# Kernel optimization log

Hardware: AMD Instinct MI355X
Metric: run time of the kernel (lower is better)

Reference implementation:

```python
import jax, jax.numpy as jnp
import numpy as np

N_NODES = 100000
N_EDGES = 600000
D = 128
L = 4
BN_EPS = 1e-5


def setup_inputs() -> dict:
    key = jax.random.key(0)
    ks = jax.random.split(key, 12)
    x = jax.random.normal(ks[0], (N_NODES, D), dtype=jnp.float32)
    edge_index = jax.random.randint(ks[1], (2, N_EDGES), 0, N_NODES, dtype=jnp.int64)
    edge_attr = jax.random.uniform(ks[2], (N_EDGES, 1), dtype=jnp.float32)
    s = 0.05
    return {
        'x': x,
        'edge_index': edge_index,
        'edge_attr': edge_attr,
        'We': jax.random.normal(ks[3], (L, 1, D), dtype=jnp.float32) * s,   # GINE edge projection Linear(1, D)
        'be': jnp.zeros((L, D), dtype=jnp.float32),
        'eps': jnp.zeros((L,), dtype=jnp.float32),                          # train_eps=True, init 0
        'W1': jax.random.normal(ks[4], (L, D, D), dtype=jnp.float32) * s,
        'b1': jnp.zeros((L, D), dtype=jnp.float32),
        'gamma': jnp.ones((L, D), dtype=jnp.float32),
        'beta': jnp.zeros((L, D), dtype=jnp.float32),
        'W2': jax.random.normal(ks[5], (L, D, D), dtype=jnp.float32) * s,
        'b2': jnp.zeros((L, D), dtype=jnp.float32),
    }


def _gine_layer(h, src, dst, edge_attr, We, be, eps, W1, b1, gamma, beta, W2, b2):
    n = h.shape[0]
    e = edge_attr @ We + be                       # [E, D] edge embedding
    m = jax.nn.relu(h[src] + e)                   # gather + add + relu (messages)
    agg = jax.ops.segment_sum(m, dst, num_segments=n)  # scatter-add to destination nodes
    z = (1.0 + eps) * h + agg
    # MLP: Linear -> BatchNorm1d (training stats) -> ReLU -> Linear
    z = z @ W1 + b1
    mu = jnp.mean(z, axis=0)
    var = jnp.var(z, axis=0)                      # biased var, as in torch BN training
    z = (z - mu) * jax.lax.rsqrt(var + BN_EPS) * gamma + beta
    z = jax.nn.relu(z)
    return z @ W2 + b2


def reference(x, edge_index, edge_attr, We, be, eps, W1, b1, gamma, beta, W2, b2):
    src, dst = edge_index[0], edge_index[1]
    h = x
    for l in range(L):
        z = _gine_layer(h, src, dst, edge_attr, We[l], be[l], eps[l],
                        W1[l], b1[l], gamma[l], beta[l], W2[l], b2[l])
        r = jax.nn.relu(z)
        h = r if l == 0 else h + r
    return h
```

## Files before the change

kernel.cpp:

```cpp
#include <hip/hip_runtime.h>

#define NN 100000
#define NE 600000
#define DD 128
#define NL 4
#define GB 512

typedef __attribute__((ext_vector_type(8))) short short8;
typedef __attribute__((ext_vector_type(4))) float float4v;

__device__ inline unsigned short f2bf(float f) {
  union { float f; unsigned u; } v; v.f = f;
  unsigned r = v.u + 0x7fff + ((v.u >> 16) & 1);
  return (unsigned short)(r >> 16);
}
__device__ inline float bf2f(unsigned short u) {
  union { unsigned u; float f; } v; v.u = ((unsigned)u) << 16;
  return v.f;
}

__global__ void k_prep(const float* __restrict__ W1, const float* __restrict__ W2,
                       unsigned short* __restrict__ WT, int* __restrict__ counts,
                       float* __restrict__ stats4) {
  int i = blockIdx.x * 256 + threadIdx.x;
  if (i < NN) counts[i] = 0;
  if (i < NL * 256) stats4[i] = 0.f;
  if (i >= 8 * 16384) return;
  int m = i >> 14;
  int el = i & 16383;
  int k = el >> 7;
  int n = el & 127;
  const float* src = (m < 4) ? (W1 + (size_t)m * 16384) : (W2 + (size_t)(m - 4) * 16384);
  WT[(size_t)m * 16384 + n * 128 + k] = f2bf(src[k * 128 + n]);
}

__global__ void k_h2b(const float* __restrict__ src, unsigned short* __restrict__ dst,
                      const int* __restrict__ ei, int* __restrict__ counts) {
  int i = blockIdx.x * 256 + threadIdx.x;
  if (i < NE) atomicAdd(&counts[ei[NE + i]], 1);
  if (i >= NN * DD / 4) return;
  float4 v = ((const float4*)src)[i];
  ushort4 o;
  o.x = f2bf(v.x); o.y = f2bf(v.y); o.z = f2bf(v.z); o.w = f2bf(v.w);
  ((ushort4*)dst)[i] = o;
}

#define ST 256
#define SC 2
#define SB ((NN + ST * SC - 1) / (ST * SC))

__global__ void k_scan_part(const int* __restrict__ counts, int* __restrict__ row_ptr,
                            int* __restrict__ bsums) {
  __shared__ int s[ST];
  int b = blockIdx.x, t = threadIdx.x;
  int base = b * (ST * SC) + t * SC;
  int v0 = (base < NN) ? counts[base] : 0;
  int v1 = (base + 1 < NN) ? counts[base + 1] : 0;
  int tsum = v0 + v1;
  s[t] = tsum;
  __syncthreads();
  for (int d = 1; d < ST; d <<= 1) {
    int x = (t >= d) ? s[t - d] : 0;
    __syncthreads();
    s[t] += x;
    __syncthreads();
  }
  int excl = s[t] - tsum;
  if (base < NN) row_ptr[base] = excl;
  if (base + 1 < NN) row_ptr[base + 1] = excl + v0;
  if (t == ST - 1) bsums[b] = s[t];
}

__global__ void k_scan_bsum(const int* __restrict__ bsums, int* __restrict__ boffs,
                            int* __restrict__ row_ptr) {
  __shared__ int s[ST];
  int t = threadIdx.x;
  int v = (t < SB) ? bsums[t] : 0;
  s[t] = v;
  __syncthreads();
  for (int d = 1; d < ST; d <<= 1) {
    int x = (t >= d) ? s[t - d] : 0;
    __syncthreads();
    s[t] += x;
    __syncthreads();
  }
  if (t < SB) boffs[t] = s[t] - v;
  if (t == ST - 1) row_ptr[NN] = s[t];
}

__global__ void k_scan_add(const int* __restrict__ boffs, int* __restrict__ row_ptr,
                           int* __restrict__ off) {
  int b = blockIdx.x, t = threadIdx.x;
  int base = b * (ST * SC) + t * SC;
  int o = boffs[b];
  if (base < NN) { row_ptr[base] += o; off[base] = 0; }
  if (base + 1 < NN) { row_ptr[base + 1] += o; off[base + 1] = 0; }
}

__global__ void k_fill(const int* __restrict__ ei, const float* __restrict__ attr,
                       const int* __restrict__ row_ptr, int* __restrict__ off,
                       int2* __restrict__ csr) {
  int e = blockIdx.x * 256 + threadIdx.x;
  if (e >= NE) return;
  int srcv = ei[e];
  int dstv = ei[NE + e];
  int pos = atomicAdd(&off[dstv], 1);
  int idx = row_ptr[dstv] + pos;
  csr[idx] = make_int2(srcv, __float_as_int(attr[e]));
}

#define CONSUME(hv, a)                                                                   \
  do {                                                                                   \
    acc0.x += fmaxf(__uint_as_float((hv).x << 16)          + fmaf((a), we0.x, be0.x), 0.f); \
    acc0.y += fmaxf(__uint_as_float((hv).x & 0xffff0000u)  + fmaf((a), we0.y, be0.y), 0.f); \
    acc0.z += fmaxf(__uint_as_float((hv).y << 16)          + fmaf((a), we0.z, be0.z), 0.f); \
    acc0.w += fmaxf(__uint_as_float((hv).y & 0xffff0000u)  + fmaf((a), we0.w, be0.w), 0.f); \
    acc1.x += fmaxf(__uint_as_float((hv).z << 16)          + fmaf((a), we1.x, be1.x), 0.f); \
    acc1.y += fmaxf(__uint_as_float((hv).z & 0xffff0000u)  + fmaf((a), we1.y, be1.y), 0.f); \
    acc1.z += fmaxf(__uint_as_float((hv).w << 16)          + fmaf((a), we1.z, be1.z), 0.f); \
    acc1.w += fmaxf(__uint_as_float((hv).w & 0xffff0000u)  + fmaf((a), we1.w, be1.w), 0.f); \
  } while (0)

__global__ void k_agg(const unsigned short* __restrict__ hb,
                      const int* __restrict__ row_ptr, const int2* __restrict__ csr,
                      const float* __restrict__ We, const float* __restrict__ be,
                      const float* __restrict__ epsp, unsigned short* __restrict__ zb) {
  int gid = blockIdx.x * blockDim.x + threadIdx.x;
  int n = gid >> 4;
  int li = gid & 15;
  if (n >= NN) return;
  int d0 = li * 8;
  float4 we0 = *(const float4*)(We + d0);
  float4 we1 = *(const float4*)(We + d0 + 4);
  float4 be0 = *(const float4*)(be + d0);
  float4 be1 = *(const float4*)(be + d0 + 4);
  int b = row_ptr[n], e = row_ptr[n + 1];
  int deg = e - b;
  int cnt = (deg < 16) ? deg : 16;
  int2 rec = (li < cnt) ? csr[b + li] : make_int2(0, 0);
  int myidx = rec.x;
  float myatt = __int_as_float(rec.y);

  float4 acc0 = make_float4(0.f, 0.f, 0.f, 0.f);
  float4 acc1 = make_float4(0.f, 0.f, 0.f, 0.f);

  int i = 0;
  for (; i + 4 <= cnt; i += 4) {
    int s0 = __shfl(myidx, i, 16);
    int s1 = __shfl(myidx, i + 1, 16);
    int s2 = __shfl(myidx, i + 2, 16);
    int s3 = __shfl(myidx, i + 3, 16);
    float a0 = __shfl(myatt, i, 16);
    float a1 = __shfl(myatt, i + 1, 16);
    float a2 = __shfl(myatt, i + 2, 16);
    float a3 = __shfl(myatt, i + 3, 16);
    uint4 hv0 = *(const uint4*)(hb + (size_t)s0 * DD + d0);
    uint4 hv1 = *(const uint4*)(hb + (size_t)s1 * DD + d0);
    uint4 hv2 = *(const uint4*)(hb + (size_t)s2 * DD + d0);
    uint4 hv3 = *(const uint4*)(hb + (size_t)s3 * DD + d0);
    CONSUME(hv0, a0);
    CONSUME(hv1, a1);
    CONSUME(hv2, a2);
    CONSUME(hv3, a3);
  }
  for (; i < cnt; i++) {
    int s = __shfl(myidx, i, 16);
    float a = __shfl(myatt, i, 16);
    uint4 hv = *(const uint4*)(hb + (size_t)s * DD + d0);
    CONSUME(hv, a);
  }
  for (int j = b + 16; j < e; j++) {
    int2 r2 = csr[j];
    float a = __int_as_float(r2.y);
    uint4 hv = *(const uint4*)(hb + (size_t)r2.x * DD + d0);
    CONSUME(hv, a);
  }

  float ep = 1.f + epsp[0];
  uint4 hs = *(const uint4*)(hb + (size_t)n * DD + d0);
  float z0 = fmaf(ep, __uint_as_float(hs.x << 16), acc0.x);
  float z1 = fmaf(ep, __uint_as_float(hs.x & 0xffff0000u), acc0.y);
  float z2 = fmaf(ep, __uint_as_float(hs.y << 16), acc0.z);
  float z3 = fmaf(ep, __uint_as_float(hs.y & 0xffff0000u), acc0.w);
  float z4 = fmaf(ep, __uint_as_float(hs.z << 16), acc1.x);
  float z5 = fmaf(ep, __uint_as_float(hs.z & 0xffff0000u), acc1.y);
  float z6 = fmaf(ep, __uint_as_float(hs.w << 16), acc1.z);
  float z7 = fmaf(ep, __uint_as_float(hs.w & 0xffff0000u), acc1.w);
  uint4 o;
  o.x = (unsigned)f2bf(z0) | ((unsigned)f2bf(z1) << 16);
  o.y = (unsigned)f2bf(z2) | ((unsigned)f2bf(z3) << 16);
  o.z = (unsigned)f2bf(z4) | ((unsigned)f2bf(z5) << 16);
  o.w = (unsigned)f2bf(z6) | ((unsigned)f2bf(z7) << 16);
  *(uint4*)(zb + (size_t)n * DD + d0) = o;
}

template <int MODE>
__global__ __launch_bounds__(256, 2) void k_gemm(
    const unsigned short* __restrict__ Xb, const unsigned short* __restrict__ WT,
    const float* __restrict__ bias, float* __restrict__ stats,
    const float* __restrict__ gamma, const float* __restrict__ beta,
    const float* __restrict__ hprev, float* __restrict__ Yout,
    unsigned short* __restrict__ Ybf) {
  __shared__ unsigned short Wl[128 * 136];
  __shared__ unsigned short Xl[2][64 * 136];
  __shared__ float bns[256];
  const int tid = threadIdx.x;
  const int G = gridDim.x;
  const int NT = (NN + 63) >> 6;

  for (int i = tid; i < 2048; i += 256) {
    int rr = i >> 4, c = i & 15;
    *(uint4*)&Wl[rr * 136 + c * 8] = *(const uint4*)&WT[rr * 128 + c * 8];
  }

  const int lane = tid & 63;
  const int w = tid >> 6;
  const int m = lane & 15;
  const int quad = lane >> 4;

  const int c8 = tid & 15, rr16 = tid >> 4;
  float scl[8], sfl[8];
  if (MODE >= 1) {
    if (tid < 128) {
      const float invN = 1.f / (float)NN;
      float mu = stats[tid] * invN;
      float var = fmaxf(stats[128 + tid] * invN - mu * mu, 0.f);
      float xx = var + 1e-5f;
      float r = rsqrtf(xx);
      r = r * (1.5f - 0.5f * xx * r * r);
      float scale = gamma[tid] * r;
      bns[tid] = scale;
      bns[128 + tid] = beta[tid] - mu * scale;
    }
    __syncthreads();
#pragma unroll
    for (int j = 0; j < 8; j++) {
      scl[j] = bns[c8 * 8 + j];
      sfl[j] = bns[128 + c8 * 8 + j];
    }
  }

  uint4 xu[4];
  auto LOADR = [&](int t) {
    int r0 = t << 6;
#pragma unroll
    for (int it = 0; it < 4; it++) {
      int gr = r0 + rr16 + it * 16;
      xu[it] = (gr < NN) ? *(const uint4*)(Xb + (size_t)gr * DD + c8 * 8)
                         : make_uint4(0u, 0u, 0u, 0u);
    }
  };
  auto STORE_LDS = [&](int b) {
#pragma unroll
    for (int it = 0; it < 4; it++) {
      int row = rr16 + it * 16;
      uint4 u = xu[it];
      if (MODE >= 1) {
        unsigned p[4] = {u.x, u.y, u.z, u.w};
#pragma unroll
        for (int j = 0; j < 4; j++) {
          float lo = bf2f((unsigned short)(p[j] & 0xffffu));
          float hi = bf2f((unsigned short)(p[j] >> 16));
          lo = fmaxf(fmaf(lo, scl[2 * j], sfl[2 * j]), 0.f);
          hi = fmaxf(fmaf(hi, scl[2 * j + 1], sfl[2 * j + 1]), 0.f);
          p[j] = (unsigned)f2bf(lo) | ((unsigned)f2bf(hi) << 16);
        }
        u = make_uint4(p[0], p[1], p[2], p[3]);
      }
      *(uint4*)&Xl[b][row * 136 + c8 * 8] = u;
    }
  };

  float4v ssum[8], ssq[8];
  if (MODE == 0) {
#pragma unroll
    for (int ct = 0; ct < 8; ct++) {
      ssum[ct] = (float4v){0.f, 0.f, 0.f, 0.f};
      ssq[ct] = (float4v){0.f, 0.f, 0.f, 0.f};
    }
  }

  const int t0 = blockIdx.x;
  LOADR(t0);
  STORE_LDS(0);
  if (t0 + G < NT) LOADR(t0 + G);
  __syncthreads();

  int buf = 0;
  for (int t = t0; t < NT; t += G) {
    const int nxt = t + G;
    if (nxt < NT) {
      STORE_LDS(buf ^ 1);
      if (nxt + G < NT) LOADR(nxt + G);
    }

    float4v acc[8];
#pragma unroll
    for (int ct = 0; ct < 8; ct++) {
      float4 b4 = *(const float4*)&bias[ct * 16 + quad * 4];
      acc[ct] = (float4v){b4.x, b4.y, b4.z, b4.w};
    }

    const unsigned short* Ap = &Wl[m * 136 + quad * 8];
    const unsigned short* Bp = &Xl[buf][(w * 16 + m) * 136 + quad * 8];
#pragma unroll
    for (int q = 0; q < 4; q++) {
      short8 bfrag = *(const short8*)(Bp + q * 32);
#pragma unroll
      for (int ct = 0; ct < 8; ct++) {
        short8 afrag = *(const short8*)(Ap + ct * 16 * 136 + q * 32);
        acc[ct] = __builtin_amdgcn_mfma_f32_16x16x32_bf16(afrag, bfrag, acc[ct], 0, 0, 0);
      }
    }

    asm volatile("s_waitcnt lgkmcnt(0)" ::: "memory");
    __builtin_amdgcn_s_barrier();

    const int r = (t << 6) + w * 16 + m;
    if (r < NN) {
      const size_t rb = (size_t)r * DD;
#pragma unroll
      for (int ct = 0; ct < 8; ct++) {
        float4v v = acc[ct];
        const int col = ct * 16 + quad * 4;
        if (MODE == 0) {
          ssum[ct] += v;
          ssq[ct] += v * v;
          ushort4 o;
          o.x = f2bf(v[0]); o.y = f2bf(v[1]); o.z = f2bf(v[2]); o.w = f2bf(v[3]);
          *(ushort4*)&Ybf[rb + col] = o;
        } else {
          v[0] = fmaxf(v[0], 0.f); v[1] = fmaxf(v[1], 0.f);
          v[2] = fmaxf(v[2], 0.f); v[3] = fmaxf(v[3], 0.f);
          if (MODE == 2) {
            float4 hp = *(const float4*)&hprev[rb + col];
            v[0] += hp.x; v[1] += hp.y; v[2] += hp.z; v[3] += hp.w;
          }
          *(float4v*)&Yout[rb + col] = v;
          if (Ybf) {
            ushort4 o;
            o.x = f2bf(v[0]); o.y = f2bf(v[1]); o.z = f2bf(v[2]); o.w = f2bf(v[3]);
            *(ushort4*)&Ybf[rb + col] = o;
          }
        }
      }
    }
    buf ^= 1;
  }

  if (MODE == 0) {
    float* sarr = (float*)Xl;
    float* sqarr = sarr + 512;
#pragma unroll
    for (int ct = 0; ct < 8; ct++) {
      float4v s = ssum[ct], s2 = ssq[ct];
#pragma unroll
      for (int d = 1; d < 16; d <<= 1) {
#pragma unroll
        for (int j = 0; j < 4; j++) {
          s[j] += __shfl_xor(s[j], d);
          s2[j] += __shfl_xor(s2[j], d);
        }
      }
      if (m == 0) {
        *(float4v*)&sarr[w * 128 + ct * 16 + quad * 4] = s;
        *(float4v*)&sqarr[w * 128 + ct * 16 + quad * 4] = s2;
      }
    }
    __syncthreads();
    if (tid < 128) {
      atomicAdd(&stats[tid], sarr[tid] + sarr[128 + tid] + sarr[256 + tid] + sarr[384 + tid]);
    } else {
      int c = tid - 128;
      atomicAdd(&stats[128 + c], sqarr[c] + sqarr[128 + c] + sqarr[256 + c] + sqarr[384 + c]);
    }
  }
}

static inline size_t align256(size_t x) { return (x + 255) & ~(size_t)255; }

extern "C" void kernel_launch(void* const* d_in, const int* in_sizes, int n_in,
                              void* d_out, int out_size, void* d_ws, size_t ws_size,
                              hipStream_t stream) {
  const float* x     = (const float*)d_in[0];
  const int*   ei    = (const int*)d_in[1];
  const float* attr  = (const float*)d_in[2];
  const float* We    = (const float*)d_in[3];
  const float* be    = (const float*)d_in[4];
  const float* eps   = (const float*)d_in[5];
  const float* W1    = (const float*)d_in[6];
  const float* b1    = (const float*)d_in[7];
  const float* gamma = (const float*)d_in[8];
  const float* beta  = (const float*)d_in[9];
  const float* W2    = (const float*)d_in[10];
  const float* b2    = (const float*)d_in[11];
  float* out = (float*)d_out;

  char* w = (char*)d_ws;
  unsigned short* z2 = (unsigned short*)w; w += align256((size_t)NN * DD * 2);
  unsigned short* hb = (unsigned short*)w; w += align256((size_t)NN * DD * 2);
  unsigned short* zb = (unsigned short*)w; w += align256((size_t)NN * DD * 2);
  int*   row_ptr  = (int*)w;   w += align256((size_t)(NN + 1) * 4);
  int*   counts   = (int*)w;   w += align256((size_t)NN * 4);
  int*   off      = (int*)w;   w += align256((size_t)NN * 4);
  int2*  csr      = (int2*)w;  w += align256((size_t)NE * 8);
  float* stats4   = (float*)w; w += align256((size_t)NL * 256 * 4);
  int*   bsums    = (int*)w;   w += align256(ST * 4);
  int*   boffs    = (int*)w;   w += align256(ST * 4);
  unsigned short* WTb = (unsigned short*)w; w += align256((size_t)8 * 16384 * 2);

  k_prep<<<512, 256, 0, stream>>>(W1, W2, WTb, counts, stats4);
  k_h2b<<<(NN * DD / 4 + 255) / 256, 256, 0, stream>>>(x, hb, ei, counts);
  k_scan_part<<<SB, ST, 0, stream>>>(counts, row_ptr, bsums);
  k_scan_bsum<<<1, ST, 0, stream>>>(bsums, boffs, row_ptr);
  k_scan_add<<<SB, ST, 0, stream>>>(boffs, row_ptr, off);
  k_fill<<<(NE + 255) / 256, 256, 0, stream>>>(ei, attr, row_ptr, off, csr);

  for (int l = 0; l < NL; l++) {
    float* st = stats4 + (size_t)l * 256;
    k_agg<<<(NN * 16 + 255) / 256, 256, 0, stream>>>(
        hb, row_ptr, csr, We + l * DD, be + l * DD, eps + l, zb);
    k_gemm<0><<<GB, 256, 0, stream>>>(zb, WTb + (size_t)l * 16384, b1 + l * DD,
                                      st, nullptr, nullptr, nullptr, nullptr, z2);
    unsigned short* hbo = (l < NL - 1) ? hb : nullptr;
    if (l == 0)
      k_gemm<1><<<GB, 256, 0, stream>>>(z2, WTb + (size_t)(4 + l) * 16384, b2 + l * DD,
                                        st, gamma + l * DD, beta + l * DD,
                                        nullptr, out, hbo);
    else
      k_gemm<2><<<GB, 256, 0, stream>>>(z2, WTb + (size_t)(4 + l) * 16384, b2 + l * DD,
                                        st, gamma + l * DD, beta + l * DD,
                                        out, out, hbo);
  }
}
```

Baseline: 532.8 us.

## Make aggregation kernel grid-stride with prefetch of next node's CSR records

The aggregation kernel now launches a fixed grid of 1024 blocks and loops over nodes grid-stride, prefetching the next node's row pointers and first 16 CSR records while the current node's messages are consumed. The per-element math is rewritten with float2 vector ops to encourage packed FP32 instructions. Separately, the scan now seeds the offset array with row starts so the fill kernel uses the atomic result directly, dropping one row_ptr load. The risk is fewer resident waves hiding gather latency, since the grid is much smaller than one thread group per node.

```diff
diff --git a/kernel.cpp b/kernel.cpp
--- a/kernel.cpp
+++ b/kernel.cpp
@@ -8,6 +8,7 @@
 
 typedef __attribute__((ext_vector_type(8))) short short8;
 typedef __attribute__((ext_vector_type(4))) float float4v;
+typedef __attribute__((ext_vector_type(2))) float f2;
 
 __device__ inline unsigned short f2bf(float f) {
   union { float f; unsigned u; } v; v.f = f;
@@ -17,6 +18,12 @@
 __device__ inline float bf2f(unsigned short u) {
   union { unsigned u; float f; } v; v.u = ((unsigned)u) << 16;
   return v.f;
+}
+__device__ inline f2 bfpair(unsigned u) {
+  f2 r;
+  r.x = __uint_as_float(u << 16);
+  r.y = __uint_as_float(u & 0xffff0000u);
+  return r;
 }
 
 __global__ void k_prep(const float* __restrict__ W1, const float* __restrict__ W2,
@@ -93,105 +100,120 @@
   int b = blockIdx.x, t = threadIdx.x;
   int base = b * (ST * SC) + t * SC;
   int o = boffs[b];
-  if (base < NN) { row_ptr[base] += o; off[base] = 0; }
-  if (base + 1 < NN) { row_ptr[base + 1] += o; off[base + 1] = 0; }
+  if (base < NN) { int v = row_ptr[base] + o; row_ptr[base] = v; off[base] = v; }
+  if (base + 1 < NN) { int v = row_ptr[base + 1] + o; row_ptr[base + 1] = v; off[base + 1] = v; }
 }
 
 __global__ void k_fill(const int* __restrict__ ei, const float* __restrict__ attr,
-                       const int* __restrict__ row_ptr, int* __restrict__ off,
-                       int2* __restrict__ csr) {
+                       int* __restrict__ off, int2* __restrict__ csr) {
   int e = blockIdx.x * 256 + threadIdx.x;
   if (e >= NE) return;
   int srcv = ei[e];
   int dstv = ei[NE + e];
-  int pos = atomicAdd(&off[dstv], 1);
-  int idx = row_ptr[dstv] + pos;
+  int idx = atomicAdd(&off[dstv], 1);
   csr[idx] = make_int2(srcv, __float_as_int(attr[e]));
 }
 
-#define CONSUME(hv, a)                                                                   \
-  do {                                                                                   \
-    acc0.x += fmaxf(__uint_as_float((hv).x << 16)          + fmaf((a), we0.x, be0.x), 0.f); \
-    acc0.y += fmaxf(__uint_as_float((hv).x & 0xffff0000u)  + fmaf((a), we0.y, be0.y), 0.f); \
-    acc0.z += fmaxf(__uint_as_float((hv).y << 16)          + fmaf((a), we0.z, be0.z), 0.f); \
-    acc0.w += fmaxf(__uint_as_float((hv).y & 0xffff0000u)  + fmaf((a), we0.w, be0.w), 0.f); \
-    acc1.x += fmaxf(__uint_as_float((hv).z << 16)          + fmaf((a), we1.x, be1.x), 0.f); \
-    acc1.y += fmaxf(__uint_as_float((hv).z & 0xffff0000u)  + fmaf((a), we1.y, be1.y), 0.f); \
-    acc1.z += fmaxf(__uint_as_float((hv).w << 16)          + fmaf((a), we1.z, be1.z), 0.f); \
-    acc1.w += fmaxf(__uint_as_float((hv).w & 0xffff0000u)  + fmaf((a), we1.w, be1.w), 0.f); \
-  } while (0)
-
-__global__ void k_agg(const unsigned short* __restrict__ hb,
-                      const int* __restrict__ row_ptr, const int2* __restrict__ csr,
-                      const float* __restrict__ We, const float* __restrict__ be,
-                      const float* __restrict__ epsp, unsigned short* __restrict__ zb) {
-  int gid = blockIdx.x * blockDim.x + threadIdx.x;
-  int n = gid >> 4;
-  int li = gid & 15;
+__global__ __launch_bounds__(256) void k_agg(
+    const unsigned short* __restrict__ hb,
+    const int* __restrict__ row_ptr, const int2* __restrict__ csr,
+    const float* __restrict__ We, const float* __restrict__ be,
+    const float* __restrict__ epsp, unsigned short* __restrict__ zb) {
+  const int tid0 = blockIdx.x * 256 + threadIdx.x;
+  const int li = tid0 & 15;
+  const int g0 = tid0 >> 4;
+  const int NG = (gridDim.x * 256) >> 4;
+  const int d0 = li * 8;
+
+  const f2 we01 = *(const f2*)(We + d0);
+  const f2 we23 = *(const f2*)(We + d0 + 2);
+  const f2 we45 = *(const f2*)(We + d0 + 4);
+  const f2 we67 = *(const f2*)(We + d0 + 6);
+  const f2 be01 = *(const f2*)(be + d0);
+  const f2 be23 = *(const f2*)(be + d0 + 2);
+  const f2 be45 = *(const f2*)(be + d0 + 4);
+  const f2 be67 = *(const f2*)(be + d0 + 6);
+  const float ep = 1.f + epsp[0];
+  f2 ep2; ep2.x = ep; ep2.y = ep;
+  const f2 zero2 = {0.f, 0.f};
+
+  int n = g0;
   if (n >= NN) return;
-  int d0 = li * 8;
-  float4 we0 = *(const float4*)(We + d0);
-  float4 we1 = *(const float4*)(We + d0 + 4);
-  float4 be0 = *(const float4*)(be + d0);
-  float4 be1 = *(const float4*)(be + d0 + 4);
   int b = row_ptr[n], e = row_ptr[n + 1];
-  int deg = e - b;
-  int cnt = (deg < 16) ? deg : 16;
+  int cnt = min(e - b, 16);
   int2 rec = (li < cnt) ? csr[b + li] : make_int2(0, 0);
-  int myidx = rec.x;
-  float myatt = __int_as_float(rec.y);
-
-  float4 acc0 = make_float4(0.f, 0.f, 0.f, 0.f);
-  float4 acc1 = make_float4(0.f, 0.f, 0.f, 0.f);
-
-  int i = 0;
-  for (; i + 4 <= cnt; i += 4) {
-    int s0 = __shfl(myidx, i, 16);
-    int s1 = __shfl(myidx, i + 1, 16);
-    int s2 = __shfl(myidx, i + 2, 16);
-    int s3 = __shfl(myidx, i + 3, 16);
-    float a0 = __shfl(myatt, i, 16);
-    float a1 = __shfl(myatt, i + 1, 16);
-    float a2 = __shfl(myatt, i + 2, 16);
-    float a3 = __shfl(myatt, i + 3, 16);
-    uint4 hv0 = *(const uint4*)(hb + (size_t)s0 * DD + d0);
-    uint4 hv1 = *(const uint4*)(hb + (size_t)s1 * DD + d0);
-    uint4 hv2 = *(const uint4*)(hb + (size_t)s2 * DD + d0);
-    uint4 hv3 = *(const uint4*)(hb + (size_t)s3 * DD + d0);
-    CONSUME(hv0, a0);
-    CONSUME(hv1, a1);
-    CONSUME(hv2, a2);
-    CONSUME(hv3, a3);
-  }
-  for (; i < cnt; i++) {
-    int s = __shfl(myidx, i, 16);
-    float a = __shfl(myatt, i, 16);
-    uint4 hv = *(const uint4*)(hb + (size_t)s * DD + d0);
-    CONSUME(hv, a);
-  }
-  for (int j = b + 16; j < e; j++) {
-    int2 r2 = csr[j];
-    float a = __int_as_float(r2.y);
-    uint4 hv = *(const uint4*)(hb + (size_t)r2.x * DD + d0);
-    CONSUME(hv, a);
-  }
-
-  float ep = 1.f + epsp[0];
-  uint4 hs = *(const uint4*)(hb + (size_t)n * DD + d0);
-  float z0 = fmaf(ep, __uint_as_float(hs.x << 16), acc0.x);
-  float z1 = fmaf(ep, __uint_as_float(hs.x & 0xffff0000u), acc0.y);
-  float z2 = fmaf(ep, __uint_as_float(hs.y << 16), acc0.z);
-  float z3 = fmaf(ep, __uint_as_float(hs.y & 0xffff0000u), acc0.w);
-  float z4 = fmaf(ep, __uint_as_float(hs.z << 16), acc1.x);
-  float z5 = fmaf(ep, __uint_as_float(hs.z & 0xffff0000u), acc1.y);
-  float z6 = fmaf(ep, __uint_as_float(hs.w << 16), acc1.z);
-  float z7 = fmaf(ep, __uint_as_float(hs.w & 0xffff0000u), acc1.w);
-  uint4 o;
-  o.x = (unsigned)f2bf(z0) | ((unsigned)f2bf(z1) << 16);
-  o.y = (unsigned)f2bf(z2) | ((unsigned)f2bf(z3) << 16);
-  o.z = (unsigned)f2bf(z4) | ((unsigned)f2bf(z5) << 16);
-  o.w = (unsigned)f2bf(z6) | ((unsigned)f2bf(z7) << 16);
-  *(uint4*)(zb + (size_t)n * DD + d0) = o;
+
+  while (n < NN) {
+    const int n2 = n + NG;
+    int b2 = 0, e2 = 0;
+    if (n2 < NN) { b2 = row_ptr[n2]; e2 = row_ptr[n2 + 1]; }
+    uint4 hs = *(const uint4*)(hb + (size_t)n * DD + d0);
+
+    const int myidx = rec.x;
+    const float myatt = __int_as_float(rec.y);
+    f2 a01 = zero2, a23 = zero2, a45 = zero2, a67 = zero2;
+
+#define CONS8(hv, at)                                                         \
+    do {                                                                      \
+      f2 av; av.x = (at); av.y = (at);                                        \
+      f2 e01 = av * we01 + be01, e23 = av * we23 + be23;                      \
+      f2 e45 = av * we45 + be45, e67 = av * we67 + be67;                      \
+      f2 s;                                                                   \
+      s = bfpair((hv).x) + e01; a01 += __builtin_elementwise_max(s, zero2);   \
+      s = bfpair((hv).y) + e23; a23 += __builtin_elementwise_max(s, zero2);   \
+      s = bfpair((hv).z) + e45; a45 += __builtin_elementwise_max(s, zero2);   \
+      s = bfpair((hv).w) + e67; a67 += __builtin_elementwise_max(s, zero2);   \
+    } while (0)
+
+    int i = 0;
+    for (; i + 4 <= cnt; i += 4) {
+      int s0 = __shfl(myidx, i, 16);
+      int s1 = __shfl(myidx, i + 1, 16);
+      int s2 = __shfl(myidx, i + 2, 16);
+      int s3 = __shfl(myidx, i + 3, 16);
+      float a0 = __shfl(myatt, i, 16);
+      float a1 = __shfl(myatt, i + 1, 16);
+      float a2 = __shfl(myatt, i + 2, 16);
+      float a3 = __shfl(myatt, i + 3, 16);
+      uint4 hv0 = *(const uint4*)(hb + (size_t)s0 * DD + d0);
+      uint4 hv1 = *(const uint4*)(hb + (size_t)s1 * DD + d0);
+      uint4 hv2 = *(const uint4*)(hb + (size_t)s2 * DD + d0);
+      uint4 hv3 = *(const uint4*)(hb + (size_t)s3 * DD + d0);
+      CONS8(hv0, a0);
+      CONS8(hv1, a1);
+      CONS8(hv2, a2);
+      CONS8(hv3, a3);
+    }
+    for (; i < cnt; i++) {
+      int s = __shfl(myidx, i, 16);
+      float a = __shfl(myatt, i, 16);
+      uint4 hv = *(const uint4*)(hb + (size_t)s * DD + d0);
+      CONS8(hv, a);
+    }
+    for (int j = b + 16; j < e; j++) {
+      int2 r2 = csr[j];
+      float a = __int_as_float(r2.y);
+      uint4 hv = *(const uint4*)(hb + (size_t)r2.x * DD + d0);
+      CONS8(hv, a);
+    }
+#undef CONS8
+
+    int cnt2 = min(e2 - b2, 16);
+    int2 rec2 = (n2 < NN && li < cnt2) ? csr[b2 + li] : make_int2(0, 0);
+
+    f2 z01 = ep2 * bfpair(hs.x) + a01;
+    f2 z23 = ep2 * bfpair(hs.y) + a23;
+    f2 z45 = ep2 * bfpair(hs.z) + a45;
+    f2 z67 = ep2 * bfpair(hs.w) + a67;
+    uint4 o;
+    o.x = (unsigned)f2bf(z01.x) | ((unsigned)f2bf(z01.y) << 16);
+    o.y = (unsigned)f2bf(z23.x) | ((unsigned)f2bf(z23.y) << 16);
+    o.z = (unsigned)f2bf(z45.x) | ((unsigned)f2bf(z45.y) << 16);
+    o.w = (unsigned)f2bf(z67.x) | ((unsigned)f2bf(z67.y) << 16);
+    *(uint4*)(zb + (size_t)n * DD + d0) = o;
+
+    n = n2; b = b2; e = e2; cnt = cnt2; rec = rec2;
+  }
 }
 
 template <int MODE>
@@ -414,11 +436,11 @@
   k_scan_part<<<SB, ST, 0, stream>>>(counts, row_ptr, bsums);
   k_scan_bsum<<<1, ST, 0, stream>>>(bsums, boffs, row_ptr);
   k_scan_add<<<SB, ST, 0, stream>>>(boffs, row_ptr, off);
-  k_fill<<<(NE + 255) / 256, 256, 0, stream>>>(ei, attr, row_ptr, off, csr);
+  k_fill<<<(NE + 255) / 256, 256, 0, stream>>>(ei, attr, off, csr);
 
   for (int l = 0; l < NL; l++) {
     float* st = stats4 + (size_t)l * 256;
-    k_agg<<<(NN * 16 + 255) / 256, 256, 0, stream>>>(
+    k_agg<<<1024, 256, 0, stream>>>(
         hb, row_ptr, csr, We + l * DD, be + l * DD, eps + l, zb);
     k_gemm<0><<<GB, 256, 0, stream>>>(zb, WTb + (size_t)l * 16384, b1 + l * DD,
                                       st, nullptr, nullptr, nullptr, nullptr, z2);
```

After: 533.5 us. About the same (+0.1%).
